# Kernel tuning notes

Hardware: AMD Instinct MI355X
Metric: run time of the kernel (lower is better)

The kernel has to match this reference:

```python
import jax, jax.numpy as jnp
import numpy as np

BETA = 0.25
N_CODEBOOK = 2  # hard-coded in the original module
EPS = 1e-12     # torch F.normalize default eps


def l2norm(t):
    # matches torch.nn.functional.normalize(t, p=2, dim=-1)
    n = jnp.linalg.norm(t, axis=-1, keepdims=True)
    return t / jnp.maximum(n, EPS)


def setup_inputs() -> dict:
    key = jax.random.key(0)
    k1, k2 = jax.random.split(key)
    b, n, e_dim, n_e = 16, 256, 1024, 4096
    c = e_dim // N_CODEBOOK
    z = jax.random.normal(k1, (b, n, e_dim), dtype=jnp.float32)
    emb_weight = jax.random.normal(k2, (N_CODEBOOK * n_e, c), dtype=jnp.float32)
    return {"z": z, "emb_weight": emb_weight}


def reference(z, emb_weight):
    b, n, e_dim = z.shape
    f = N_CODEBOOK
    c = e_dim // f
    n_e = emb_weight.shape[0] // f

    # 'b n (f c) -> b f n c'
    zf = jnp.transpose(z.reshape(b, n, f, c), (0, 2, 1, 3))
    # '(b f) c -> b f c' with b=2 (codebooks), f=n_e
    protos = emb_weight.reshape(f, n_e, c)

    zn = l2norm(zf)            # (b, f, n, c)
    pn = l2norm(protos)        # (f, m, c)

    # cosine distance; batch repeat of prototypes is a pure broadcast
    d = 2.0 - 2.0 * jnp.einsum('bfnc,fmc->bfnm', zn, pn)  # (b, f, n, m)
    encoding_indices = jnp.argmin(d, axis=-1)              # (b, f, n) in [0, n_e)

    # faithful to source: indices gather from the FULL (2*n_e) table, no offset
    z_q = l2norm(emb_weight[encoding_indices])             # (b, f, n, c)

    sg = jax.lax.stop_gradient
    loss = BETA * jnp.mean((sg(z_q) - zn) ** 2) + jnp.mean((z_q - sg(zn)) ** 2)

    z_q_st = zn + sg(z_q - zn)                             # straight-through
    # 'b f n c -> b n (f c)'
    z_q_out = jnp.transpose(z_q_st, (0, 2, 1, 3)).reshape(b, n, e_dim)
    return z_q_out, loss, encoding_indices
```

## Files before the change

### kernel.cpp

```cpp
#include <hip/hip_runtime.h>
#include <hip/hip_bf16.h>
#include <stdint.h>

#define FCB 2
#define BB 16
#define NN 256
#define EDIM 1024
#define CC 512
#define NE 4096
#define TOKENS (BB*FCB*NN)
#define ROWS (FCB*NE)
#define OUT_LOSS (BB*NN*EDIM)
#define OUT_IDX  (OUT_LOSS + 1)
#define MARGIN 0.15f

typedef __attribute__((ext_vector_type(8))) short bf16x8;
typedef __attribute__((ext_vector_type(4))) float f32x4;

__device__ __forceinline__ unsigned int ford(float v) {
    unsigned int u = __float_as_uint(v);
    return (u & 0x80000000u) ? ~u : (u | 0x80000000u);
}
__device__ __forceinline__ float unford(unsigned int u) {
    unsigned int b = (u & 0x80000000u) ? (u & 0x7fffffffu) : ~u;
    return __uint_as_float(b);
}


__global__ __launch_bounds__(256) void init_kernel(
    const float* __restrict__ emb, float* __restrict__ inv_norm)
{
    int r = blockIdx.x;
    int tid = threadIdx.x;
    const float* row = emb + (size_t)r * CC;
    float a = row[tid], b = row[tid + 256];
    float ss = a*a + b*b;
    #pragma unroll
    for (int off = 32; off; off >>= 1) ss += __shfl_down(ss, off);
    __shared__ float part[4];
    if ((tid & 63) == 0) part[tid >> 6] = ss;
    __syncthreads();
    if (tid == 0) {
        float t = part[0] + part[1] + part[2] + part[3];
        inv_norm[r] = 1.0f / fmaxf(sqrtf(t), 1e-12f);
    }
}

__global__ __launch_bounds__(256) void pack_hi(
    const float* __restrict__ z, const float* __restrict__ emb,
    short* __restrict__ z_hi, short* __restrict__ e_hi)
{
    int bid = blockIdx.x;
    const float* src; short* hi; int RS, FRO, FCO;
    if (bid < 2048) { src = z;   hi = z_hi; RS = EDIM; FRO = 0;  FCO = CC; }
    else            { src = emb; hi = e_hi; RS = CC;   FRO = NE; FCO = 0; bid -= 2048; }
    int u = bid * 256 + threadIdx.x;
    int m = u & 15;
    int Q = (u >> 4) & 63;
    int R = (u >> 10) & 255;
    int f = u >> 18;
    int row = R * 16 + m;
    const float* s = src + (size_t)(f * FRO + row) * RS + f * FCO + Q * 8;
    float4 v0 = *(const float4*)s;
    float4 v1 = *(const float4*)(s + 4);
    float vv[8] = {v0.x, v0.y, v0.z, v0.w, v1.x, v1.y, v1.z, v1.w};
    bf16x8 h8;
    #pragma unroll
    for (int j = 0; j < 8; ++j) {
        __hip_bfloat16 hb = __float2bfloat16(vv[j]);
        h8[j] = *(short*)&hb;
    }
    *(bf16x8*)(hi + (size_t)u * 8) = h8;
}

__global__ __launch_bounds__(256, 3) void gemm_sel(
    const short* __restrict__ zh, const short* __restrict__ eh,
    const float* __restrict__ inv_norm, unsigned long long* __restrict__ cand)
{
    __shared__ char smem[16384];
    const int f  = blockIdx.z;
    const int t0 = blockIdx.y * 128;
    const int m0 = blockIdx.x * 128;
    const int tid  = threadIdx.x;
    const int wave = tid >> 6, lane = tid & 63;
    const int wm = wave & 1, wn = wave >> 1;

    f32x4 acc[4][4] = {};

    for (int step = 0; step < 16; ++step) {
        const int qb = step * 4;
        __syncthreads();
        #pragma unroll
        for (int i = 0; i < 4; ++i) {
            int c = wave * 4 + i;
            const short* gsrc = (c < 8) ? zh : eh;
            int R = (c < 8) ? ((t0 >> 4) + c) : ((m0 >> 4) + (c - 8));
            const short* g = gsrc
                + (((size_t)f * 256 + R) * 64 + qb) * 128 + (size_t)lane * 8;
            __builtin_amdgcn_global_load_lds(
                (const __attribute__((address_space(1))) void*)g,
                (__attribute__((address_space(3))) void*)(smem + c * 1024),
                16, 0, 0);
        }
        __syncthreads();

        bf16x8 ah[4], bh[4];
        #pragma unroll
        for (int i = 0; i < 4; ++i) {
            ah[i] = *(const bf16x8*)(smem + (wm * 4 + i) * 1024 + lane * 16);
            bh[i] = *(const bf16x8*)(smem + 8192 + (wn * 4 + i) * 1024 + lane * 16);
        }
        #pragma unroll
        for (int i = 0; i < 4; ++i)
            #pragma unroll
            for (int j2 = 0; j2 < 4; ++j2)
                acc[i][j2] = __builtin_amdgcn_mfma_f32_16x16x32_bf16(ah[i], bh[j2], acc[i][j2], 0, 0, 0);
    }

    float inm[4]; int nid[4];
    #pragma unroll
    for (int j2 = 0; j2 < 4; ++j2) {
        nid[j2] = m0 + wn * 64 + j2 * 16 + (lane & 15);
        inm[j2] = inv_norm[f * NE + nid[j2]];
    }

    #pragma unroll
    for (int i = 0; i < 4; ++i) {
        #pragma unroll
        for (int r = 0; r < 4; ++r) {
            unsigned long long p1 = 0ull, p2 = 0ull;
            #pragma unroll
            for (int j2 = 0; j2 < 4; ++j2) {
                float w = acc[i][j2][r] * inm[j2];
                unsigned long long pw = ((unsigned long long)ford(w) << 32)
                                      | (unsigned int)(~(unsigned int)nid[j2]);
                if (pw > p1) { p2 = p1; p1 = pw; }
                else if (pw > p2) p2 = pw;
            }
            #pragma unroll
            for (int off = 8; off; off >>= 1) {
                unsigned long long q1 = __shfl_down(p1, off, 16);
                unsigned long long q2 = __shfl_down(p2, off, 16);
                if (q1 > p1) { unsigned long long t = p1; p1 = q1; p2 = (t > q2) ? t : q2; }
                else         { p2 = (p2 > q1) ? p2 : q1; }
            }
            if ((lane & 15) == 0) {
                int u = t0 + wm * 64 + i * 16 + (lane >> 4) * 4 + r;
                int b = u >> 8, n = u & 255;
                int gt = ((b * FCB + f) << 8) + n;
                unsigned long long* slot =
                    cand + (((size_t)gt << 6) + (blockIdx.x << 1) + wn) * 2;
                slot[0] = p1; slot[1] = p2;
            }
        }
    }
}

__global__ __launch_bounds__(256) void rescore_epilogue(
    const float* __restrict__ z, const float* __restrict__ emb,
    const float* __restrict__ inv_norm, const unsigned long long* __restrict__ cand,
    float* __restrict__ out, float* __restrict__ loss_tok)
{
    int t = blockIdx.x * 4 + (threadIdx.x >> 6);
    int lane = threadIdx.x & 63;
    int n = t & 255;
    int f = (t >> 8) & 1;
    int b = t >> 9;
    const float* zrow = z + ((size_t)(b*NN + n))*EDIM + f*CC;
    float4 za = *(const float4*)(zrow + lane * 8);
    float4 zb = *(const float4*)(zrow + lane * 8 + 4);

    const unsigned long long* slot = cand + (((size_t)t << 6) + lane) * 2;
    unsigned long long c1 = slot[0], c2 = slot[1];

    unsigned long long m1 = (c1 > c2) ? c1 : c2;
    #pragma unroll
    for (int off = 32; off; off >>= 1) {
        unsigned long long o = __shfl_xor(m1, off);
        if (o > m1) m1 = o;
    }
    float vmax = unford((unsigned int)(m1 >> 32));
    float thr = vmax - MARGIN;

    unsigned long long bestp = 0ull;
    #pragma unroll
    for (int rnd = 0; rnd < 2; ++rnd) {
        unsigned long long p = rnd ? c2 : c1;
        float v = unford((unsigned int)(p >> 32));
        unsigned long long mask = __ballot(v > thr);
        while (mask) {
            int src = __ffsll((long long)mask) - 1;
            mask &= mask - 1;
            unsigned long long cp = __shfl(p, src);
            int idx = (int)(~(unsigned int)cp);
            const float* er = emb + ((size_t)(f * NE + idx)) * CC;
            float4 ea = *(const float4*)(er + lane * 8);
            float4 eb = *(const float4*)(er + lane * 8 + 4);
            float d = za.x*ea.x + za.y*ea.y + za.z*ea.z + za.w*ea.w
                    + zb.x*eb.x + zb.y*eb.y + zb.z*eb.z + zb.w*eb.w;
            #pragma unroll
            for (int off = 32; off; off >>= 1) d += __shfl_xor(d, off);
            float vex = d * inv_norm[f * NE + idx];
            unsigned long long pex = ((unsigned long long)ford(vex) << 32)
                                   | (unsigned int)(~(unsigned int)idx);
            if (pex > bestp) bestp = pex;
        }
    }
    int idxb = (int)(~(unsigned int)bestp);

    const float* er0 = emb + (size_t)idxb * CC;
    float inm0 = inv_norm[idxb];
    float* orow = out + ((size_t)(b*NN + n))*EDIM + f*CC;
    float4 ea = *(const float4*)(er0 + lane * 8);
    float4 eb = *(const float4*)(er0 + lane * 8 + 4);
    ea.x *= inm0; ea.y *= inm0; ea.z *= inm0; ea.w *= inm0;
    eb.x *= inm0; eb.y *= inm0; eb.z *= inm0; eb.w *= inm0;
    *(float4*)(orow + lane * 8) = ea;
    *(float4*)(orow + lane * 8 + 4) = eb;
    float s1 = za.x*za.x + za.y*za.y + za.z*za.z + za.w*za.w
             + zb.x*zb.x + zb.y*zb.y + zb.z*zb.z + zb.w*zb.w;
    float s2 = za.x*ea.x + za.y*ea.y + za.z*ea.z + za.w*ea.w
             + zb.x*eb.x + zb.y*eb.y + zb.z*eb.z + zb.w*eb.w;
    #pragma unroll
    for (int off = 32; off; off >>= 1) {
        s1 += __shfl_xor(s1, off);
        s2 += __shfl_xor(s2, off);
    }
    if (lane == 0) {
        float cosv = s2 / fmaxf(sqrtf(s1), 1e-12f);
        loss_tok[t] = 2.0f - 2.0f * cosv;
        out[OUT_IDX + t] = (float)idxb;
    }
}

__global__ __launch_bounds__(256) void loss_reduce(
    const float* __restrict__ loss_tok, float* __restrict__ out)
{
    int tid = threadIdx.x;
    float s = 0.f;
    #pragma unroll
    for (int h = 0; h < 32; ++h) s += loss_tok[h * 256 + tid];
    #pragma unroll
    for (int off = 32; off; off >>= 1) s += __shfl_down(s, off);
    __shared__ float part[4];
    if ((tid & 63) == 0) part[tid >> 6] = s;
    __syncthreads();
    if (tid == 0) {
        float t = part[0] + part[1] + part[2] + part[3];
        out[OUT_LOSS] = t * (1.25f / (float)OUT_LOSS);
    }
}

extern "C" void kernel_launch(void* const* d_in, const int* in_sizes, int n_in,
                              void* d_out, int out_size, void* d_ws, size_t ws_size,
                              hipStream_t stream) {
    const float* z   = (const float*)d_in[0];
    const float* emb = (const float*)d_in[1];
    float* out = (float*)d_out;

    char* ws = (char*)d_ws;
    float* inv_norm = (float*)ws;
    unsigned long long* cand = (unsigned long long*)(ws + 32768);
    float* loss_tok = (float*)(ws + 32768 + (size_t)8*1024*1024);
    short* z_hi = (short*)(ws + 65536 + (size_t)8*1024*1024);
    short* e_hi = z_hi + (size_t)FCB * NE * CC;

    init_kernel<<<ROWS, 256, 0, stream>>>(emb, inv_norm);
    pack_hi<<<4096, 256, 0, stream>>>(z, emb, z_hi, e_hi);
    gemm_sel<<<dim3(NE/128, NE/128, FCB), 256, 0, stream>>>(z_hi, e_hi, inv_norm, cand);
    rescore_epilogue<<<TOKENS/4, 256, 0, stream>>>(z, emb, inv_norm, cand, out, loss_tok);
    loss_reduce<<<1, 256, 0, stream>>>(loss_tok, out);
}
```

Measured before the change: 162.8 us.

## Fuse codebook norms into pack, double K-tile, compact 32-bit candidates

Drops the separate inverse-norm kernel. Codebook row sum-of-squares is now accumulated inside the bf16 pack kernel via shared reduction and atomics, and the GEMM applies rsqrt itself. The GEMM K-step doubles, staging 32 KB of LDS per iteration and halving the number of barrier pairs. Candidate entries shrink from 64-bit to 32-bit by packing a 6-bit local column code into the low bits of the ordered score. This halves candidate traffic, but the rescore kernel must now recompute codebook norms from the fp32 rows, and the score keeps slightly less precision.

```diff
diff --git a/kernel.cpp b/kernel.cpp
--- a/kernel.cpp
+++ b/kernel.cpp
@@ -27,34 +27,19 @@
 }
 
 
-__global__ __launch_bounds__(256) void init_kernel(
-    const float* __restrict__ emb, float* __restrict__ inv_norm)
-{
-    int r = blockIdx.x;
-    int tid = threadIdx.x;
-    const float* row = emb + (size_t)r * CC;
-    float a = row[tid], b = row[tid + 256];
-    float ss = a*a + b*b;
-    #pragma unroll
-    for (int off = 32; off; off >>= 1) ss += __shfl_down(ss, off);
-    __shared__ float part[4];
-    if ((tid & 63) == 0) part[tid >> 6] = ss;
-    __syncthreads();
-    if (tid == 0) {
-        float t = part[0] + part[1] + part[2] + part[3];
-        inv_norm[r] = 1.0f / fmaxf(sqrtf(t), 1e-12f);
-    }
-}
-
 __global__ __launch_bounds__(256) void pack_hi(
     const float* __restrict__ z, const float* __restrict__ emb,
-    short* __restrict__ z_hi, short* __restrict__ e_hi)
-{
+    short* __restrict__ z_hi, short* __restrict__ e_hi,
+    float* __restrict__ norm_sq)
+{
+    __shared__ float red[256];
     int bid = blockIdx.x;
+    int tid = threadIdx.x;
+    bool is_emb = (bid >= 2048);
     const float* src; short* hi; int RS, FRO, FCO;
-    if (bid < 2048) { src = z;   hi = z_hi; RS = EDIM; FRO = 0;  FCO = CC; }
-    else            { src = emb; hi = e_hi; RS = CC;   FRO = NE; FCO = 0; bid -= 2048; }
-    int u = bid * 256 + threadIdx.x;
+    if (!is_emb) { src = z;   hi = z_hi; RS = EDIM; FRO = 0;  FCO = CC; }
+    else         { src = emb; hi = e_hi; RS = CC;   FRO = NE; FCO = 0; bid -= 2048; }
+    int u = bid * 256 + tid;
     int m = u & 15;
     int Q = (u >> 4) & 63;
     int R = (u >> 10) & 255;
@@ -65,19 +50,34 @@
     float4 v1 = *(const float4*)(s + 4);
     float vv[8] = {v0.x, v0.y, v0.z, v0.w, v1.x, v1.y, v1.z, v1.w};
     bf16x8 h8;
+    float ss = 0.f;
     #pragma unroll
     for (int j = 0; j < 8; ++j) {
         __hip_bfloat16 hb = __float2bfloat16(vv[j]);
         h8[j] = *(short*)&hb;
+        ss = fmaf(vv[j], vv[j], ss);
     }
     *(bf16x8*)(hi + (size_t)u * 8) = h8;
+
+    if (is_emb) {
+        red[tid] = ss;
+        __syncthreads();
+        if (tid < 16) {
+            float t = 0.f;
+            #pragma unroll
+            for (int q = 0; q < 16; ++q) t += red[tid + 16 * q];
+            int bf = (bid * 256) >> 18;
+            int bR = ((bid * 256) >> 10) & 255;
+            atomicAdd(norm_sq + bf * NE + bR * 16 + tid, t);
+        }
+    }
 }
 
 __global__ __launch_bounds__(256, 3) void gemm_sel(
     const short* __restrict__ zh, const short* __restrict__ eh,
-    const float* __restrict__ inv_norm, unsigned long long* __restrict__ cand)
-{
-    __shared__ char smem[16384];
+    const float* __restrict__ norm_sq, unsigned int* __restrict__ cand)
+{
+    __shared__ char smem[32768];
     const int f  = blockIdx.z;
     const int t0 = blockIdx.y * 128;
     const int m0 = blockIdx.x * 128;
@@ -87,14 +87,16 @@
 
     f32x4 acc[4][4] = {};
 
-    for (int step = 0; step < 16; ++step) {
-        const int qb = step * 4;
+    for (int step = 0; step < 8; ++step) {
         __syncthreads();
         #pragma unroll
-        for (int i = 0; i < 4; ++i) {
-            int c = wave * 4 + i;
-            const short* gsrc = (c < 8) ? zh : eh;
-            int R = (c < 8) ? ((t0 >> 4) + c) : ((m0 >> 4) + (c - 8));
+        for (int i = 0; i < 8; ++i) {
+            int c = wave * 8 + i;
+            const short* gsrc = (c < 16) ? zh : eh;
+            int cl = c & 15;
+            int Rl = cl >> 1, h = cl & 1;
+            int R = ((c < 16) ? (t0 >> 4) : (m0 >> 4)) + Rl;
+            int qb = step * 8 + h * 4;
             const short* g = gsrc
                 + (((size_t)f * 256 + R) * 64 + qb) * 128 + (size_t)lane * 8;
             __builtin_amdgcn_global_load_lds(
@@ -104,53 +106,56 @@
         }
         __syncthreads();
 
-        bf16x8 ah[4], bh[4];
         #pragma unroll
-        for (int i = 0; i < 4; ++i) {
-            ah[i] = *(const bf16x8*)(smem + (wm * 4 + i) * 1024 + lane * 16);
-            bh[i] = *(const bf16x8*)(smem + 8192 + (wn * 4 + i) * 1024 + lane * 16);
-        }
-        #pragma unroll
-        for (int i = 0; i < 4; ++i)
-            #pragma unroll
-            for (int j2 = 0; j2 < 4; ++j2)
-                acc[i][j2] = __builtin_amdgcn_mfma_f32_16x16x32_bf16(ah[i], bh[j2], acc[i][j2], 0, 0, 0);
-    }
-
-    float inm[4]; int nid[4];
+        for (int h = 0; h < 2; ++h) {
+            bf16x8 ah[4], bh[4];
+            #pragma unroll
+            for (int i = 0; i < 4; ++i) {
+                ah[i] = *(const bf16x8*)(smem + ((wm*4 + i)*2 + h) * 1024 + lane * 16);
+                bh[i] = *(const bf16x8*)(smem + 16384 + ((wn*4 + i)*2 + h) * 1024 + lane * 16);
+            }
+            #pragma unroll
+            for (int i = 0; i < 4; ++i)
+                #pragma unroll
+                for (int j2 = 0; j2 < 4; ++j2)
+                    acc[i][j2] = __builtin_amdgcn_mfma_f32_16x16x32_bf16(ah[i], bh[j2], acc[i][j2], 0, 0, 0);
+        }
+    }
+
+    float inm[4]; unsigned ccode[4];
     #pragma unroll
     for (int j2 = 0; j2 < 4; ++j2) {
-        nid[j2] = m0 + wn * 64 + j2 * 16 + (lane & 15);
-        inm[j2] = inv_norm[f * NE + nid[j2]];
+        int col = j2 * 16 + (lane & 15);
+        ccode[j2] = (unsigned)(col ^ 63);
+        inm[j2] = rsqrtf(norm_sq[f * NE + m0 + wn * 64 + col]);
     }
 
     #pragma unroll
     for (int i = 0; i < 4; ++i) {
         #pragma unroll
         for (int r = 0; r < 4; ++r) {
-            unsigned long long p1 = 0ull, p2 = 0ull;
+            unsigned p1 = 0u, p2 = 0u;
             #pragma unroll
             for (int j2 = 0; j2 < 4; ++j2) {
                 float w = acc[i][j2][r] * inm[j2];
-                unsigned long long pw = ((unsigned long long)ford(w) << 32)
-                                      | (unsigned int)(~(unsigned int)nid[j2]);
+                unsigned pw = (ford(w) & 0xFFFFFFC0u) | ccode[j2];
                 if (pw > p1) { p2 = p1; p1 = pw; }
                 else if (pw > p2) p2 = pw;
             }
             #pragma unroll
             for (int off = 8; off; off >>= 1) {
-                unsigned long long q1 = __shfl_down(p1, off, 16);
-                unsigned long long q2 = __shfl_down(p2, off, 16);
-                if (q1 > p1) { unsigned long long t = p1; p1 = q1; p2 = (t > q2) ? t : q2; }
+                unsigned q1 = __shfl_down(p1, off, 16);
+                unsigned q2 = __shfl_down(p2, off, 16);
+                if (q1 > p1) { unsigned t = p1; p1 = q1; p2 = (t > q2) ? t : q2; }
                 else         { p2 = (p2 > q1) ? p2 : q1; }
             }
             if ((lane & 15) == 0) {
                 int u = t0 + wm * 64 + i * 16 + (lane >> 4) * 4 + r;
                 int b = u >> 8, n = u & 255;
                 int gt = ((b * FCB + f) << 8) + n;
-                unsigned long long* slot =
-                    cand + (((size_t)gt << 6) + (blockIdx.x << 1) + wn) * 2;
-                slot[0] = p1; slot[1] = p2;
+                int s = (blockIdx.x << 1) | wn;
+                uint2 val; val.x = p1; val.y = p2;
+                *(uint2*)(cand + ((size_t)gt << 7) + (s << 1)) = val;
             }
         }
     }
@@ -158,7 +163,7 @@
 
 __global__ __launch_bounds__(256) void rescore_epilogue(
     const float* __restrict__ z, const float* __restrict__ emb,
-    const float* __restrict__ inv_norm, const unsigned long long* __restrict__ cand,
+    const unsigned int* __restrict__ cand,
     float* __restrict__ out, float* __restrict__ loss_tok)
 {
     int t = blockIdx.x * 4 + (threadIdx.x >> 6);
@@ -170,37 +175,41 @@
     float4 za = *(const float4*)(zrow + lane * 8);
     float4 zb = *(const float4*)(zrow + lane * 8 + 4);
 
-    const unsigned long long* slot = cand + (((size_t)t << 6) + lane) * 2;
-    unsigned long long c1 = slot[0], c2 = slot[1];
-
-    unsigned long long m1 = (c1 > c2) ? c1 : c2;
+    uint2 cc = *(const uint2*)(cand + ((size_t)t << 7) + (lane << 1));
+    unsigned c1 = cc.x, c2 = cc.y;
+
+    unsigned m1 = (c1 > c2) ? c1 : c2;
     #pragma unroll
     for (int off = 32; off; off >>= 1) {
-        unsigned long long o = __shfl_xor(m1, off);
+        unsigned o = __shfl_xor(m1, off);
         if (o > m1) m1 = o;
     }
-    float vmax = unford((unsigned int)(m1 >> 32));
-    float thr = vmax - MARGIN;
+    float thr = unford(m1) - MARGIN;
 
     unsigned long long bestp = 0ull;
     #pragma unroll
     for (int rnd = 0; rnd < 2; ++rnd) {
-        unsigned long long p = rnd ? c2 : c1;
-        float v = unford((unsigned int)(p >> 32));
+        unsigned u = rnd ? c2 : c1;
+        float v = unford(u);
         unsigned long long mask = __ballot(v > thr);
         while (mask) {
             int src = __ffsll((long long)mask) - 1;
             mask &= mask - 1;
-            unsigned long long cp = __shfl(p, src);
-            int idx = (int)(~(unsigned int)cp);
+            unsigned cu = __shfl(u, src);
+            int idx = (src << 6) | ((int)(cu & 63u) ^ 63);
             const float* er = emb + ((size_t)(f * NE + idx)) * CC;
             float4 ea = *(const float4*)(er + lane * 8);
             float4 eb = *(const float4*)(er + lane * 8 + 4);
-            float d = za.x*ea.x + za.y*ea.y + za.z*ea.z + za.w*ea.w
-                    + zb.x*eb.x + zb.y*eb.y + zb.z*eb.z + zb.w*eb.w;
-            #pragma unroll
-            for (int off = 32; off; off >>= 1) d += __shfl_xor(d, off);
-            float vex = d * inv_norm[f * NE + idx];
+            float d  = za.x*ea.x + za.y*ea.y + za.z*ea.z + za.w*ea.w
+                     + zb.x*eb.x + zb.y*eb.y + zb.z*eb.z + zb.w*eb.w;
+            float se = ea.x*ea.x + ea.y*ea.y + ea.z*ea.z + ea.w*ea.w
+                     + eb.x*eb.x + eb.y*eb.y + eb.z*eb.z + eb.w*eb.w;
+            #pragma unroll
+            for (int off = 32; off; off >>= 1) {
+                d  += __shfl_xor(d, off);
+                se += __shfl_xor(se, off);
+            }
+            float vex = d / fmaxf(sqrtf(se), 1e-12f);
             unsigned long long pex = ((unsigned long long)ford(vex) << 32)
                                    | (unsigned int)(~(unsigned int)idx);
             if (pex > bestp) bestp = pex;
@@ -209,10 +218,14 @@
     int idxb = (int)(~(unsigned int)bestp);
 
     const float* er0 = emb + (size_t)idxb * CC;
-    float inm0 = inv_norm[idxb];
-    float* orow = out + ((size_t)(b*NN + n))*EDIM + f*CC;
     float4 ea = *(const float4*)(er0 + lane * 8);
     float4 eb = *(const float4*)(er0 + lane * 8 + 4);
+    float se0 = ea.x*ea.x + ea.y*ea.y + ea.z*ea.z + ea.w*ea.w
+              + eb.x*eb.x + eb.y*eb.y + eb.z*eb.z + eb.w*eb.w;
+    #pragma unroll
+    for (int off = 32; off; off >>= 1) se0 += __shfl_xor(se0, off);
+    float inm0 = 1.0f / fmaxf(sqrtf(se0), 1e-12f);
+    float* orow = out + ((size_t)(b*NN + n))*EDIM + f*CC;
     ea.x *= inm0; ea.y *= inm0; ea.z *= inm0; ea.w *= inm0;
     eb.x *= inm0; eb.y *= inm0; eb.z *= inm0; eb.w *= inm0;
     *(float4*)(orow + lane * 8) = ea;
@@ -259,15 +272,15 @@
     float* out = (float*)d_out;
 
     char* ws = (char*)d_ws;
-    float* inv_norm = (float*)ws;
-    unsigned long long* cand = (unsigned long long*)(ws + 32768);
-    float* loss_tok = (float*)(ws + 32768 + (size_t)8*1024*1024);
-    short* z_hi = (short*)(ws + 65536 + (size_t)8*1024*1024);
+    float* norm_sq = (float*)ws;
+    unsigned int* cand = (unsigned int*)(ws + 32768);
+    float* loss_tok = (float*)(ws + 32768 + (size_t)4*1024*1024);
+    short* z_hi = (short*)(ws + 65536 + (size_t)4*1024*1024);
     short* e_hi = z_hi + (size_t)FCB * NE * CC;
 
-    init_kernel<<<ROWS, 256, 0, stream>>>(emb, inv_norm);
-    pack_hi<<<4096, 256, 0, stream>>>(z, emb, z_hi, e_hi);
-    gemm_sel<<<dim3(NE/128, NE/128, FCB), 256, 0, stream>>>(z_hi, e_hi, inv_norm, cand);
-    rescore_epilogue<<<TOKENS/4, 256, 0, stream>>>(z, emb, inv_norm, cand, out, loss_tok);
+    hipMemsetAsync(norm_sq, 0, ROWS * sizeof(float), stream);
+    pack_hi<<<4096, 256, 0, stream>>>(z, emb, z_hi, e_hi, norm_sq);
+    gemm_sel<<<dim3(NE/128, NE/128, FCB), 256, 0, stream>>>(z_hi, e_hi, norm_sq, cand);
+    rescore_epilogue<<<TOKENS/4, 256, 0, stream>>>(z, emb, cand, out, loss_tok);
     loss_reduce<<<1, 256, 0, stream>>>(loss_tok, out);
 }
```

Result: faster. 143.2 us (-12.0%).
